# Kernel optimization log

Measured on AMD Instinct MI355X. Metric: run time of the kernel, lower is better.

Reference implementation:

```python
import jax, jax.numpy as jnp
import numpy as np

N = 100000          # nodes
E = 1600000         # edges
IN_F = 128          # in_features
OUT_F = 64          # attention_dim = out_features
H = 8               # heads
D_K = OUT_F // H    # 8


def setup_inputs() -> dict:
    key = jax.random.key(0)
    ks = jax.random.split(key, 8)
    x = jax.random.normal(ks[0], (N, IN_F), dtype=jnp.float32)
    edge = jax.random.randint(ks[1], (2, E), 0, N, dtype=jnp.int64)
    # Linear weights stored torch-style [out, in]; biases [out].
    Wq = jax.random.normal(ks[2], (OUT_F, IN_F), dtype=jnp.float32) * 0.02
    bq = jax.random.normal(ks[3], (OUT_F,), dtype=jnp.float32) * 0.02
    Wk = jax.random.normal(ks[4], (OUT_F, IN_F), dtype=jnp.float32) * 0.02
    bk = jax.random.normal(ks[5], (OUT_F,), dtype=jnp.float32) * 0.02
    Wv = jax.random.normal(ks[6], (OUT_F, IN_F), dtype=jnp.float32) * 0.02
    bv = jax.random.normal(ks[7], (OUT_F,), dtype=jnp.float32) * 0.02
    return {"x": x, "edge": edge, "Wq": Wq, "bq": bq, "Wk": Wk, "bk": bk, "Wv": Wv, "bv": bv}


def _segment_softmax(scores, seg_ids, num_segments):
    # scores: [E, H], seg_ids: [E]; stable softmax grouped by seg_ids
    seg_max = jax.ops.segment_max(scores, seg_ids, num_segments=num_segments)  # [N, H]
    seg_max = jnp.where(jnp.isfinite(seg_max), seg_max, 0.0)
    ex = jnp.exp(scores - seg_max[seg_ids])                                    # [E, H]
    denom = jax.ops.segment_sum(ex, seg_ids, num_segments=num_segments)        # [N, H]
    return ex / (denom[seg_ids] + 1e-16)


def reference(x, edge, Wq, bq, Wk, bk, Wv, bv):
    src_idx = edge[0]  # source node per edge (softmax group + output row)
    dst_idx = edge[1]  # destination node per edge (k/v gather)

    q = (x @ Wq.T + bq).reshape(N, H, D_K)  # [N, H, D_K]
    k = (x @ Wk.T + bk).reshape(N, H, D_K)
    v = (x @ Wv.T + bv).reshape(N, H, D_K)

    # per-edge dot-product attention scores over d_k
    prods = jnp.sum(q[src_idx] * k[dst_idx], axis=-1) / np.sqrt(D_K)  # [E, H]
    attn = _segment_softmax(prods, src_idx, N)                         # [E, H]

    # spmm per head, vectorized: out[i] = sum_{e: src=i} attn[e,h] * v[dst[e],h,:]
    msgs = attn[:, :, None] * v[dst_idx]                               # [E, H, D_K]
    out = jax.ops.segment_sum(msgs, src_idx, num_segments=N)           # [N, H, D_K]
    # head-major concat matches torch loop-concat of [N, D_K] blocks
    return out.reshape(N, H * D_K)
```

## Files before the change

### kernel.cpp

```cpp
#include <hip/hip_runtime.h>

#define N_NODES   100000
#define E_EDGES   1600000
#define IN_FEATS  128
#define OUT_FEATS 64
#define NH        8
#define DK        8

#define QKV_BLOCKS   782
#define CSTR         32
#define CAP          64
#define E4           (E_EDGES / 4)
#define CNT4         (N_NODES * CSTR / 4)

typedef __attribute__((ext_vector_type(8))) short short8;
typedef __attribute__((ext_vector_type(4))) float floatx4;

__device__ __forceinline__ ushort f2bf(float f) {
    uint u = __float_as_uint(f);
    u += 0x7FFF + ((u >> 16) & 1);
    return (ushort)(u >> 16);
}
__device__ __forceinline__ float bflo(uint u) { return __uint_as_float(u << 16); }
__device__ __forceinline__ float bfhi(uint u) { return __uint_as_float(u & 0xFFFF0000u); }

__global__ __launch_bounds__(256) void prep_kernel(
    const float* __restrict__ Wq, const float* __restrict__ Wk,
    const float* __restrict__ Wv, ushort* __restrict__ Wb,
    int* __restrict__ cnt)
{
    const int i = blockIdx.x * 256 + threadIdx.x;
    if (i < CNT4) ((int4*)cnt)[i] = make_int4(0, 0, 0, 0);
    if (i < 3072) {
        const int m  = i >> 10;
        const int kc = (i >> 8) & 3;
        const int qd = (i >> 6) & 3;
        const int nt = (i >> 4) & 3;
        const int lm = i & 15;
        const float* W = (m == 0) ? Wq : (m == 1) ? Wk : Wv;
        const float* s = W + (16 * nt + lm) * IN_FEATS + 32 * kc + 8 * qd;
        const float4 f0 = ((const float4*)s)[0];
        const float4 f1 = ((const float4*)s)[1];
        ushort r[8];
        r[0] = f2bf(f0.x); r[1] = f2bf(f0.y); r[2] = f2bf(f0.z); r[3] = f2bf(f0.w);
        r[4] = f2bf(f1.x); r[5] = f2bf(f1.y); r[6] = f2bf(f1.z); r[7] = f2bf(f1.w);
        const int di = (kc >> 1) * 1536 + m * 512 + (kc & 1) * 256 + qd * 64 + nt * 16 + lm;
        *(short8*)(Wb + (size_t)di * 8) = *(short8*)r;
    }
}

__global__ __launch_bounds__(512) void qkv_hist_kernel(
    const float* __restrict__ x, const ushort* __restrict__ Wb,
    const float* __restrict__ bq, const float* __restrict__ bk,
    const float* __restrict__ bv,
    float* __restrict__ qo, uint* __restrict__ kvo,
    const int* __restrict__ src, const int* __restrict__ dst,
    int* __restrict__ cnt, int* __restrict__ csr)
{
    __shared__ short8 wlds[1536];

    if (blockIdx.x & 1) {
        const int i = (blockIdx.x >> 1) * 512 + threadIdx.x;
        if (i < E4) {
            const int4 s4 = ((const int4*)src)[i];
            const int4 d4 = ((const int4*)dst)[i];
            const int px = atomicAdd(&cnt[s4.x * CSTR], 1);
            const int py = atomicAdd(&cnt[s4.y * CSTR], 1);
            const int pz = atomicAdd(&cnt[s4.z * CSTR], 1);
            const int pw = atomicAdd(&cnt[s4.w * CSTR], 1);
            if (px < CAP) csr[s4.x * CAP + px] = d4.x;
            if (py < CAP) csr[s4.y * CAP + py] = d4.y;
            if (pz < CAP) csr[s4.z * CAP + pz] = d4.z;
            if (pw < CAP) csr[s4.w * CAP + pw] = d4.w;
        }
        return;
    }

    const int t    = threadIdx.x;
    const int lane = t & 63;
    const int w    = t >> 6;
    const int lm   = lane & 15;
    const int qd   = lane >> 4;
    const int row0 = (blockIdx.x >> 1) * 128 + 16 * w;

    #pragma unroll
    for (int c = 0; c < 3; ++c) {
        const int i = t + 512 * c;
        wlds[i] = *(const short8*)(Wb + (size_t)i * 8);
    }

    const int  arow   = row0 + lm;
    const bool avalid = arow < N_NODES;
    short8 afrag[4];
    #pragma unroll
    for (int kc = 0; kc < 4; ++kc) {
        float4 f0 = make_float4(0.f, 0.f, 0.f, 0.f);
        float4 f1 = f0;
        if (avalid) {
            const float4* xp =
                (const float4*)(x + (size_t)arow * IN_FEATS + kc * 32 + qd * 8);
            f0 = xp[0];
            f1 = xp[1];
        }
        short8 a;
        a[0] = (short)f2bf(f0.x); a[1] = (short)f2bf(f0.y);
        a[2] = (short)f2bf(f0.z); a[3] = (short)f2bf(f0.w);
        a[4] = (short)f2bf(f1.x); a[5] = (short)f2bf(f1.y);
        a[6] = (short)f2bf(f1.z); a[7] = (short)f2bf(f1.w);
        afrag[kc] = a;
    }

    floatx4 qacc[4], kacc[4], vacc[4];
    #pragma unroll
    for (int nt = 0; nt < 4; ++nt) {
        const float bbq = bq[16 * nt + lm];
        const float bbk = bk[16 * nt + lm];
        const float bbv = bv[16 * nt + lm];
        qacc[nt] = (floatx4){bbq, bbq, bbq, bbq};
        kacc[nt] = (floatx4){bbk, bbk, bbk, bbk};
        vacc[nt] = (floatx4){bbv, bbv, bbv, bbv};
    }

    __syncthreads();

    #pragma unroll
    for (int kc = 0; kc < 2; ++kc) {
        const int fb = (kc & 1) * 256 + qd * 64 + lm;
        #pragma unroll
        for (int nt = 0; nt < 4; ++nt) {
            const short8 bq8 = wlds[fb + nt * 16];
            const short8 bk8 = wlds[fb + nt * 16 + 512];
            const short8 bv8 = wlds[fb + nt * 16 + 1024];
            qacc[nt] = __builtin_amdgcn_mfma_f32_16x16x32_bf16(afrag[kc], bq8, qacc[nt], 0, 0, 0);
            kacc[nt] = __builtin_amdgcn_mfma_f32_16x16x32_bf16(afrag[kc], bk8, kacc[nt], 0, 0, 0);
            vacc[nt] = __builtin_amdgcn_mfma_f32_16x16x32_bf16(afrag[kc], bv8, vacc[nt], 0, 0, 0);
        }
    }

    __syncthreads();

    #pragma unroll
    for (int c = 0; c < 3; ++c) {
        const int i = t + 512 * c;
        wlds[i] = *(const short8*)(Wb + (size_t)(1536 + i) * 8);
    }

    __syncthreads();

    #pragma unroll
    for (int kc = 2; kc < 4; ++kc) {
        const int fb = (kc & 1) * 256 + qd * 64 + lm;
        #pragma unroll
        for (int nt = 0; nt < 4; ++nt) {
            const short8 bq8 = wlds[fb + nt * 16];
            const short8 bk8 = wlds[fb + nt * 16 + 512];
            const short8 bv8 = wlds[fb + nt * 16 + 1024];
            qacc[nt] = __builtin_amdgcn_mfma_f32_16x16x32_bf16(afrag[kc], bq8, qacc[nt], 0, 0, 0);
            kacc[nt] = __builtin_amdgcn_mfma_f32_16x16x32_bf16(afrag[kc], bk8, kacc[nt], 0, 0, 0);
            vacc[nt] = __builtin_amdgcn_mfma_f32_16x16x32_bf16(afrag[kc], bv8, vacc[nt], 0, 0, 0);
        }
    }

    #pragma unroll
    for (int nt = 0; nt < 4; ++nt) {
        #pragma unroll
        for (int reg = 0; reg < 4; ++reg) {
            const int row = row0 + 4 * qd + reg;
            if (row < N_NODES) {
                qo[(size_t)row * OUT_FEATS + 16 * nt + lm] = qacc[nt][reg];
                const uint kb = f2bf(kacc[nt][reg]);
                const uint vb = f2bf(vacc[nt][reg]);
                kvo[(size_t)row * OUT_FEATS + 16 * nt + lm] = kb | (vb << 16);
            }
        }
    }
}

__global__ __launch_bounds__(256) void attn_kernel(
    const float* __restrict__ q, const uint* __restrict__ kv,
    const int* __restrict__ cnt, const int* __restrict__ csr,
    float* __restrict__ out)
{
    const int lane = threadIdx.x & 63;
    const int wv   = threadIdx.x >> 6;
    const int node = blockIdx.x * 4 + wv;
    const int h    = lane >> 3;
    const int jme  = lane & 7;

    const float4* qrow = (const float4*)(q + (size_t)node * OUT_FEATS + h * DK);
    const float4 qa = qrow[0];
    const float4 qb = qrow[1];

    int deg = cnt[node * CSTR];
    deg = deg < CAP ? deg : CAP;

    int dn_lane = 0;
    if (lane < deg) dn_lane = csr[node * CAP + lane];

    float den = 0.f;
    float a0 = 0.f, a1 = 0.f, a2 = 0.f, a3 = 0.f;
    float a4 = 0.f, a5 = 0.f, a6 = 0.f, a7 = 0.f;

    int g = 0;
    for (; g + 16 <= deg; g += 16) {
        const int dnA = __shfl(dn_lane, g + jme);
        const int dnB = __shfl(dn_lane, g + 8 + jme);
        const uint4* kpA = (const uint4*)(kv + (size_t)dnA * OUT_FEATS + h * DK);
        const uint4* kpB = (const uint4*)(kv + (size_t)dnB * OUT_FEATS + h * DK);
        const uint4 uaA = kpA[0];
        const uint4 ubA = kpA[1];
        const uint4 uaB = kpB[0];
        const uint4 ubB = kpB[1];

        float pA = qa.x * bflo(uaA.x) + qa.y * bflo(uaA.y) +
                   qa.z * bflo(uaA.z) + qa.w * bflo(uaA.w) +
                   qb.x * bflo(ubA.x) + qb.y * bflo(ubA.y) +
                   qb.z * bflo(ubA.z) + qb.w * bflo(ubA.w);
        float pB = qa.x * bflo(uaB.x) + qa.y * bflo(uaB.y) +
                   qa.z * bflo(uaB.z) + qa.w * bflo(uaB.w) +
                   qb.x * bflo(ubB.x) + qb.y * bflo(ubB.y) +
                   qb.z * bflo(ubB.z) + qb.w * bflo(ubB.w);
        const float exA = exp2f(pA * 0.51006971413f);
        const float exB = exp2f(pB * 0.51006971413f);

        den += exA;
        a0 += exA * bfhi(uaA.x); a1 += exA * bfhi(uaA.y);
        a2 += exA * bfhi(uaA.z); a3 += exA * bfhi(uaA.w);
        a4 += exA * bfhi(ubA.x); a5 += exA * bfhi(ubA.y);
        a6 += exA * bfhi(ubA.z); a7 += exA * bfhi(ubA.w);
        den += exB;
        a0 += exB * bfhi(uaB.x); a1 += exB * bfhi(uaB.y);
        a2 += exB * bfhi(uaB.z); a3 += exB * bfhi(uaB.w);
        a4 += exB * bfhi(ubB.x); a5 += exB * bfhi(ubB.y);
        a6 += exB * bfhi(ubB.z); a7 += exB * bfhi(ubB.w);
    }
    for (; g < deg; g += 8) {
        const int dn = __shfl(dn_lane, g + jme);
        const uint4* kvp = (const uint4*)(kv + (size_t)dn * OUT_FEATS + h * DK);
        const uint4 ua = kvp[0];
        const uint4 ub = kvp[1];

        float p = qa.x * bflo(ua.x) + qa.y * bflo(ua.y) +
                  qa.z * bflo(ua.z) + qa.w * bflo(ua.w) +
                  qb.x * bflo(ub.x) + qb.y * bflo(ub.y) +
                  qb.z * bflo(ub.z) + qb.w * bflo(ub.w);
        float ex = exp2f(p * 0.51006971413f);
        if (g + jme >= deg) ex = 0.f;

        den += ex;
        a0 += ex * bfhi(ua.x); a1 += ex * bfhi(ua.y);
        a2 += ex * bfhi(ua.z); a3 += ex * bfhi(ua.w);
        a4 += ex * bfhi(ub.x); a5 += ex * bfhi(ub.y);
        a6 += ex * bfhi(ub.z); a7 += ex * bfhi(ub.w);
    }

    #pragma unroll
    for (int m = 1; m <= 4; m <<= 1) {
        den += __shfl_xor(den, m);
        a0 += __shfl_xor(a0, m); a1 += __shfl_xor(a1, m);
        a2 += __shfl_xor(a2, m); a3 += __shfl_xor(a3, m);
        a4 += __shfl_xor(a4, m); a5 += __shfl_xor(a5, m);
        a6 += __shfl_xor(a6, m); a7 += __shfl_xor(a7, m);
    }

    float r = a0;
    r = (jme == 1) ? a1 : r;
    r = (jme == 2) ? a2 : r;
    r = (jme == 3) ? a3 : r;
    r = (jme == 4) ? a4 : r;
    r = (jme == 5) ? a5 : r;
    r = (jme == 6) ? a6 : r;
    r = (jme == 7) ? a7 : r;

    out[(size_t)node * OUT_FEATS + lane] = r / (den + 1e-16f);
}

extern "C" void kernel_launch(void* const* d_in, const int* in_sizes, int n_in,
                              void* d_out, int out_size, void* d_ws, size_t ws_size,
                              hipStream_t stream)
{
    const float* x  = (const float*)d_in[0];
    const int*  edge = (const int*)d_in[1];
    const float* Wq = (const float*)d_in[2];
    const float* bq = (const float*)d_in[3];
    const float* Wk = (const float*)d_in[4];
    const float* bk = (const float*)d_in[5];
    const float* Wv = (const float*)d_in[6];
    const float* bv = (const float*)d_in[7];
    float* out = (float*)d_out;

    float* q  = (float*)d_ws;
    uint*  kv = (uint*)(q + (size_t)N_NODES * OUT_FEATS);
    int* cnt   = (int*)(kv + (size_t)N_NODES * OUT_FEATS);
    ushort* Wb = (ushort*)(cnt + (size_t)N_NODES * CSTR);
    int* csr   = (int*)(Wb + 3 * 64 * IN_FEATS);

    const int* src = edge;
    const int* dst = edge + E_EDGES;

    prep_kernel<<<(CNT4 + 255) / 256, 256, 0, stream>>>(Wq, Wk, Wv, Wb, cnt);

    qkv_hist_kernel<<<QKV_BLOCKS * 2, 512, 0, stream>>>(
        x, Wb, bq, bk, bv, q, kv, src, dst, cnt, csr);

    attn_kernel<<<N_NODES / 4, 256, 0, stream>>>(q, kv, cnt, csr, out);
}
```

Baseline: 259.6 us.

## Replace per-node counters with CAS open-addressed CSR slots and ballot compaction

Drops the padded per-node count array and atomicAdd. Each edge now claims a slot in its source node's 64-entry row by atomicCAS on a -1 sentinel, starting from a hashed position and probing linearly. The attention kernel reads the whole row, finds valid entries with a ballot and popcount, and compacts them with ds_permute. This removes the counter array, its zeroing and one dependent load. In exchange, prep must now fill the full 100000x64 CSR with -1, and CAS retries can pile up when several edges hit the same row.

Result: faster. 249.8 us (-3.8%).

```diff
diff --git a/kernel.cpp b/kernel.cpp
--- a/kernel.cpp
+++ b/kernel.cpp
@@ -8,10 +8,9 @@
 #define DK        8
 
 #define QKV_BLOCKS   782
-#define CSTR         32
 #define CAP          64
 #define E4           (E_EDGES / 4)
-#define CNT4         (N_NODES * CSTR / 4)
+#define CSRI4        (N_NODES * CAP / 4)
 
 typedef __attribute__((ext_vector_type(8))) short short8;
 typedef __attribute__((ext_vector_type(4))) float floatx4;
@@ -27,10 +26,10 @@
 __global__ __launch_bounds__(256) void prep_kernel(
     const float* __restrict__ Wq, const float* __restrict__ Wk,
     const float* __restrict__ Wv, ushort* __restrict__ Wb,
-    int* __restrict__ cnt)
+    int* __restrict__ csr)
 {
     const int i = blockIdx.x * 256 + threadIdx.x;
-    if (i < CNT4) ((int4*)cnt)[i] = make_int4(0, 0, 0, 0);
+    if (i < CSRI4) ((int4*)csr)[i] = make_int4(-1, -1, -1, -1);
     if (i < 3072) {
         const int m  = i >> 10;
         const int kc = (i >> 8) & 3;
@@ -55,7 +54,7 @@
     const float* __restrict__ bv,
     float* __restrict__ qo, uint* __restrict__ kvo,
     const int* __restrict__ src, const int* __restrict__ dst,
-    int* __restrict__ cnt, int* __restrict__ csr)
+    int* __restrict__ csr)
 {
     __shared__ short8 wlds[1536];
 
@@ -64,14 +63,32 @@
         if (i < E4) {
             const int4 s4 = ((const int4*)src)[i];
             const int4 d4 = ((const int4*)dst)[i];
-            const int px = atomicAdd(&cnt[s4.x * CSTR], 1);
-            const int py = atomicAdd(&cnt[s4.y * CSTR], 1);
-            const int pz = atomicAdd(&cnt[s4.z * CSTR], 1);
-            const int pw = atomicAdd(&cnt[s4.w * CSTR], 1);
-            if (px < CAP) csr[s4.x * CAP + px] = d4.x;
-            if (py < CAP) csr[s4.y * CAP + py] = d4.y;
-            if (pz < CAP) csr[s4.z * CAP + pz] = d4.z;
-            if (pw < CAP) csr[s4.w * CAP + pw] = d4.w;
+            const int s[4] = {s4.x, s4.y, s4.z, s4.w};
+            const int d[4] = {d4.x, d4.y, d4.z, d4.w};
+            int  slot[4];
+            bool pend[4];
+            #pragma unroll
+            for (int c = 0; c < 4; ++c) {
+                slot[c] = (4 * i + c) & (CAP - 1);
+                pend[c] = true;
+            }
+            for (int t = 0; t < CAP; ++t) {
+                bool any = false;
+                #pragma unroll
+                for (int c = 0; c < 4; ++c) {
+                    if (pend[c]) {
+                        const int prev = atomicCAS(
+                            &csr[(size_t)s[c] * CAP + slot[c]], -1, d[c]);
+                        if (prev == -1) {
+                            pend[c] = false;
+                        } else {
+                            slot[c] = (slot[c] + 1) & (CAP - 1);
+                            any = true;
+                        }
+                    }
+                }
+                if (!any) break;
+            }
         }
         return;
     }
@@ -178,8 +195,7 @@
 
 __global__ __launch_bounds__(256) void attn_kernel(
     const float* __restrict__ q, const uint* __restrict__ kv,
-    const int* __restrict__ cnt, const int* __restrict__ csr,
-    float* __restrict__ out)
+    const int* __restrict__ csr, float* __restrict__ out)
 {
     const int lane = threadIdx.x & 63;
     const int wv   = threadIdx.x >> 6;
@@ -191,11 +207,13 @@
     const float4 qa = qrow[0];
     const float4 qb = qrow[1];
 
-    int deg = cnt[node * CSTR];
-    deg = deg < CAP ? deg : CAP;
-
-    int dn_lane = 0;
-    if (lane < deg) dn_lane = csr[node * CAP + lane];
+    const int raw = csr[(size_t)node * CAP + lane];
+    const bool valid = raw >= 0;
+    const unsigned long long mask = __ballot(valid);
+    const int deg = __popcll(mask);
+    const int pv  = __popcll(mask & ((1ull << lane) - 1ull));
+    const int target = valid ? pv : (deg + (lane - pv));
+    const int dn_lane = __builtin_amdgcn_ds_permute(target << 2, valid ? raw : 0);
 
     float den = 0.f;
     float a0 = 0.f, a1 = 0.f, a2 = 0.f, a3 = 0.f;
@@ -291,17 +309,16 @@
 
     float* q  = (float*)d_ws;
     uint*  kv = (uint*)(q + (size_t)N_NODES * OUT_FEATS);
-    int* cnt   = (int*)(kv + (size_t)N_NODES * OUT_FEATS);
-    ushort* Wb = (ushort*)(cnt + (size_t)N_NODES * CSTR);
+    ushort* Wb = (ushort*)(kv + (size_t)N_NODES * OUT_FEATS);
     int* csr   = (int*)(Wb + 3 * 64 * IN_FEATS);
 
     const int* src = edge;
     const int* dst = edge + E_EDGES;
 
-    prep_kernel<<<(CNT4 + 255) / 256, 256, 0, stream>>>(Wq, Wk, Wv, Wb, cnt);
+    prep_kernel<<<(CSRI4 + 255) / 256, 256, 0, stream>>>(Wq, Wk, Wv, Wb, csr);
 
     qkv_hist_kernel<<<QKV_BLOCKS * 2, 512, 0, stream>>>(
-        x, Wb, bq, bk, bv, q, kv, src, dst, cnt, csr);
-
-    attn_kernel<<<N_NODES / 4, 256, 0, stream>>>(q, kv, cnt, csr, out);
-}
+        x, Wb, bq, bk, bv, q, kv, src, dst, csr);
+
+    attn_kernel<<<N_NODES / 4, 256, 0, stream>>>(q, kv, csr, out);
+}
```

## Replace per-node atomic CSR build with two-pass region bucketing and local sort

Applied to the files above, without the earlier changes.

Replaces the per-edge global atomics into a padded per-node counter array with a two-level scheme. Edges are first bucketed into 512-node regions using shared-memory histograms and one global atomic per region per block. A second kernel then counting-sorts each region in LDS into a dense per-node CSR with offsets and degrees. This removes the large zeroing of the padded counter array and the heavy contention from global atomics. In exchange it adds two extra kernel launches and an intermediate buffer, and it drops the previous overlap of histogram work with the QKV projection.

Measured after the change: 216.8 us. -16.5%, faster.

```diff
diff --git a/kernel.cpp b/kernel.cpp
--- a/kernel.cpp
+++ b/kernel.cpp
@@ -7,11 +7,13 @@
 #define NH        8
 #define DK        8
 
-#define QKV_BLOCKS   782
-#define CSTR         32
-#define CAP          64
-#define E4           (E_EDGES / 4)
-#define CNT4         (N_NODES * CSTR / 4)
+#define QKV_BLOCKS 782
+#define E4         (E_EDGES / 4)
+
+#define REGIONS    196
+#define RCAP       8960
+#define SC_BLOCKS  391
+#define RC_STRIDE  16
 
 typedef __attribute__((ext_vector_type(8))) short short8;
 typedef __attribute__((ext_vector_type(4))) float floatx4;
@@ -27,10 +29,10 @@
 __global__ __launch_bounds__(256) void prep_kernel(
     const float* __restrict__ Wq, const float* __restrict__ Wk,
     const float* __restrict__ Wv, ushort* __restrict__ Wb,
-    int* __restrict__ cnt)
+    uint* __restrict__ rcount)
 {
     const int i = blockIdx.x * 256 + threadIdx.x;
-    if (i < CNT4) ((int4*)cnt)[i] = make_int4(0, 0, 0, 0);
+    if (i < REGIONS * RC_STRIDE) rcount[i] = 0;
     if (i < 3072) {
         const int m  = i >> 10;
         const int kc = (i >> 8) & 3;
@@ -49,39 +51,132 @@
     }
 }
 
-__global__ __launch_bounds__(512) void qkv_hist_kernel(
+__global__ __launch_bounds__(512) void scatter_kernel(
+    const int* __restrict__ src, const int* __restrict__ dst,
+    uint* __restrict__ rcount, uint* __restrict__ seg)
+{
+    __shared__ uint hist[REGIONS];
+    __shared__ uint gbase[REGIONS];
+
+    const int tid = threadIdx.x;
+    const int gt  = blockIdx.x * 512 + tid;
+
+    if (tid < REGIONS) hist[tid] = 0;
+    __syncthreads();
+
+    int sv[8], dv[8], loc[8];
+    int nv = 0;
+    #pragma unroll
+    for (int p = 0; p < 2; ++p) {
+        const int qi = gt * 2 + p;
+        if (qi < E4) {
+            const int4 s4 = ((const int4*)src)[qi];
+            const int4 d4 = ((const int4*)dst)[qi];
+            sv[p * 4 + 0] = s4.x; sv[p * 4 + 1] = s4.y;
+            sv[p * 4 + 2] = s4.z; sv[p * 4 + 3] = s4.w;
+            dv[p * 4 + 0] = d4.x; dv[p * 4 + 1] = d4.y;
+            dv[p * 4 + 2] = d4.z; dv[p * 4 + 3] = d4.w;
+            nv = p * 4 + 4;
+        }
+    }
+
+    #pragma unroll
+    for (int e = 0; e < 8; ++e) {
+        if (e < nv) loc[e] = (int)atomicAdd(&hist[sv[e] >> 9], 1u);
+    }
+    __syncthreads();
+
+    if (tid < REGIONS) {
+        const uint h = hist[tid];
+        gbase[tid] = h ? atomicAdd(&rcount[tid * RC_STRIDE], h) : 0u;
+    }
+    __syncthreads();
+
+    #pragma unroll
+    for (int e = 0; e < 8; ++e) {
+        if (e < nv) {
+            const int  r   = sv[e] >> 9;
+            const uint pos = gbase[r] + (uint)loc[e];
+            if (pos < RCAP)
+                seg[(size_t)r * RCAP + pos] =
+                    (uint)dv[e] | ((uint)(sv[e] & 511) << 17);
+        }
+    }
+}
+
+__global__ __launch_bounds__(512) void build_kernel(
+    const uint* __restrict__ rcount, const uint* __restrict__ seg,
+    uint* __restrict__ dense, int* __restrict__ node_off,
+    int* __restrict__ degw)
+{
+    __shared__ uint ec[RCAP];
+    __shared__ uint cnt[512];
+    __shared__ uint cnt2[512];
+    __shared__ uint off[512];
+    __shared__ uint wsum[8];
+
+    const int r    = blockIdx.x;
+    const int tid  = threadIdx.x;
+    const int lane = tid & 63;
+    const int wid  = tid >> 6;
+    const int n0   = r << 9;
+
+    int m = (int)rcount[r * RC_STRIDE];
+    if (m > RCAP) m = RCAP;
+
+    cnt[tid]  = 0;
+    cnt2[tid] = 0;
+    for (int i = tid; i < m; i += 512) ec[i] = seg[(size_t)r * RCAP + i];
+    __syncthreads();
+
+    for (int i = tid; i < m; i += 512) atomicAdd(&cnt[ec[i] >> 17], 1u);
+    __syncthreads();
+
+    const uint v = cnt[tid];
+    uint inc = v;
+    #pragma unroll
+    for (int d = 1; d < 64; d <<= 1) {
+        const uint t = __shfl_up(inc, d);
+        if (lane >= d) inc += t;
+    }
+    if (lane == 63) wsum[wid] = inc;
+    __syncthreads();
+    if (tid == 0) {
+        uint a = 0;
+        #pragma unroll
+        for (int w2 = 0; w2 < 8; ++w2) { const uint t = wsum[w2]; wsum[w2] = a; a += t; }
+    }
+    __syncthreads();
+    off[tid] = inc - v + wsum[wid];
+    __syncthreads();
+
+    for (int i = tid; i < m; i += 512) {
+        const uint s = ec[i] >> 17;
+        const uint p = off[s] + atomicAdd(&cnt2[s], 1u);
+        dense[(size_t)r * RCAP + p] = ec[i] & 0x1FFFFu;
+    }
+
+    const int node = n0 + tid;
+    if (node < N_NODES) {
+        node_off[node] = r * RCAP + (int)off[tid];
+        degw[node]     = (int)cnt[tid];
+    }
+}
+
+__global__ __launch_bounds__(512) void qkv_kernel(
     const float* __restrict__ x, const ushort* __restrict__ Wb,
     const float* __restrict__ bq, const float* __restrict__ bk,
     const float* __restrict__ bv,
-    float* __restrict__ qo, uint* __restrict__ kvo,
-    const int* __restrict__ src, const int* __restrict__ dst,
-    int* __restrict__ cnt, int* __restrict__ csr)
+    float* __restrict__ qo, uint* __restrict__ kvo)
 {
     __shared__ short8 wlds[1536];
-
-    if (blockIdx.x & 1) {
-        const int i = (blockIdx.x >> 1) * 512 + threadIdx.x;
-        if (i < E4) {
-            const int4 s4 = ((const int4*)src)[i];
-            const int4 d4 = ((const int4*)dst)[i];
-            const int px = atomicAdd(&cnt[s4.x * CSTR], 1);
-            const int py = atomicAdd(&cnt[s4.y * CSTR], 1);
-            const int pz = atomicAdd(&cnt[s4.z * CSTR], 1);
-            const int pw = atomicAdd(&cnt[s4.w * CSTR], 1);
-            if (px < CAP) csr[s4.x * CAP + px] = d4.x;
-            if (py < CAP) csr[s4.y * CAP + py] = d4.y;
-            if (pz < CAP) csr[s4.z * CAP + pz] = d4.z;
-            if (pw < CAP) csr[s4.w * CAP + pw] = d4.w;
-        }
-        return;
-    }
 
     const int t    = threadIdx.x;
     const int lane = t & 63;
     const int w    = t >> 6;
     const int lm   = lane & 15;
     const int qd   = lane >> 4;
-    const int row0 = (blockIdx.x >> 1) * 128 + 16 * w;
+    const int row0 = blockIdx.x * 128 + 16 * w;
 
     #pragma unroll
     for (int c = 0; c < 3; ++c) {
@@ -178,8 +273,8 @@
 
 __global__ __launch_bounds__(256) void attn_kernel(
     const float* __restrict__ q, const uint* __restrict__ kv,
-    const int* __restrict__ cnt, const int* __restrict__ csr,
-    float* __restrict__ out)
+    const uint* __restrict__ dense, const int* __restrict__ node_off,
+    const int* __restrict__ degw, float* __restrict__ out)
 {
     const int lane = threadIdx.x & 63;
     const int wv   = threadIdx.x >> 6;
@@ -191,11 +286,12 @@
     const float4 qa = qrow[0];
     const float4 qb = qrow[1];
 
-    int deg = cnt[node * CSTR];
-    deg = deg < CAP ? deg : CAP;
+    const int offn = node_off[node];
+    int deg = degw[node];
+    deg = deg < 64 ? deg : 64;
 
     int dn_lane = 0;
-    if (lane < deg) dn_lane = csr[node * CAP + lane];
+    if (lane < deg) dn_lane = (int)dense[(size_t)offn + lane];
 
     float den = 0.f;
     float a0 = 0.f, a1 = 0.f, a2 = 0.f, a3 = 0.f;
@@ -289,19 +385,25 @@
     const float* bv = (const float*)d_in[7];
     float* out = (float*)d_out;
 
-    float* q  = (float*)d_ws;
-    uint*  kv = (uint*)(q + (size_t)N_NODES * OUT_FEATS);
-    int* cnt   = (int*)(kv + (size_t)N_NODES * OUT_FEATS);
-    ushort* Wb = (ushort*)(cnt + (size_t)N_NODES * CSTR);
-    int* csr   = (int*)(Wb + 3 * 64 * IN_FEATS);
+    float*  q        = (float*)d_ws;
+    uint*   kv       = (uint*)(q + (size_t)N_NODES * OUT_FEATS);
+    ushort* Wb       = (ushort*)(kv + (size_t)N_NODES * OUT_FEATS);
+    uint*   rcount   = (uint*)(Wb + 3 * 64 * IN_FEATS);
+    uint*   seg      = rcount + REGIONS * RC_STRIDE;
+    uint*   dense    = seg + (size_t)REGIONS * RCAP;
+    int*    node_off = (int*)(dense + (size_t)REGIONS * RCAP);
+    int*    degw     = node_off + N_NODES;
 
     const int* src = edge;
     const int* dst = edge + E_EDGES;
 
-    prep_kernel<<<(CNT4 + 255) / 256, 256, 0, stream>>>(Wq, Wk, Wv, Wb, cnt);
-
-    qkv_hist_kernel<<<QKV_BLOCKS * 2, 512, 0, stream>>>(
-        x, Wb, bq, bk, bv, q, kv, src, dst, cnt, csr);
-
-    attn_kernel<<<N_NODES / 4, 256, 0, stream>>>(q, kv, cnt, csr, out);
-}
+    prep_kernel<<<13, 256, 0, stream>>>(Wq, Wk, Wv, Wb, rcount);
+
+    scatter_kernel<<<SC_BLOCKS, 512, 0, stream>>>(src, dst, rcount, seg);
+
+    build_kernel<<<REGIONS, 512, 0, stream>>>(rcount, seg, dense, node_off, degw);
+
+    qkv_kernel<<<QKV_BLOCKS, 512, 0, stream>>>(x, Wb, bq, bk, bv, q, kv);
+
+    attn_kernel<<<N_NODES / 4, 256, 0, stream>>>(q, kv, dense, node_off, degw, out);
+}
```
